# Kernel tuning notes

Hardware: AMD Instinct MI355X
Metric: run time of the kernel (lower is better)

The kernel has to match this reference:

```python
import jax, jax.numpy as jnp
import numpy as np

B, IN, OUT = 128, 1024, 1024
BETA, THRESHOLD, RESET = 0.99, 1.0, 0.8
TAU_POS, TAU_NEG = 20.0, 20.0
A_POS, A_NEG = 0.005, 0.005


def setup_inputs() -> dict:
    key = jax.random.key(0)
    k1, k2, k3, k4, k5 = jax.random.split(key, 5)
    in_spikes = (jax.random.uniform(k1, (B, IN)) < 0.1).astype(jnp.float32)
    # nn.Linear default init: U(-1/sqrt(in), 1/sqrt(in))
    bound = 1.0 / np.sqrt(IN)
    W = jax.random.uniform(k2, (OUT, IN), minval=-bound, maxval=bound, dtype=jnp.float32)
    membrane = jax.random.normal(k3, (B, OUT), dtype=jnp.float32) * 0.5
    # trace timers (time since last spike), random in [0, 50)
    delta_pre = jax.random.uniform(k4, (B, IN), dtype=jnp.float32) * 50.0
    delta_fire = jax.random.uniform(k5, (B, OUT), dtype=jnp.float32) * 50.0
    return {"in_spikes": in_spikes, "W": W, "membrane": membrane,
            "delta_pre": delta_pre, "delta_fire": delta_fire}


def reference(in_spikes, W, membrane, delta_pre, delta_fire):
    # dense projection (bias is unused in the original forward)
    weighted = jnp.matmul(in_spikes, W.T)                      # (B, OUT)
    # LIF neuron
    mem = membrane * BETA + weighted
    spike = (mem > THRESHOLD).astype(jnp.float32)
    mem = jnp.where(spike > 0, mem - RESET, mem)
    # trace updates: increment, reset-to-zero where a spike occurred
    dp = jnp.where(in_spikes > 0, 0.0, delta_pre + 1.0)        # (B, IN)
    df = jnp.where(spike > 0, 0.0, delta_fire + 1.0)           # (B, OUT)
    # pairwise timing difference: (B, IN, OUT)
    delta_t = df[:, None, :] - dp[:, :, None]
    potentiation = (delta_t > 0) * (A_POS * jnp.exp(-delta_t / TAU_POS))
    depression = (delta_t < 0) * (A_NEG * jnp.exp(delta_t / TAU_NEG))
    weight_changes = potentiation - depression                 # (B, IN, OUT)
    avg_weight_changes = weight_changes.mean(axis=0).T         # (OUT, IN)
    new_W = W + avg_weight_changes
    return spike, new_W, mem
```

## Files before the change

### kernel.cpp

```cpp
#include <hip/hip_runtime.h>
#include <cstdint>
#include <cmath>

#define Bb   128
#define INN  1024
#define OUTN 1024
#define A_TOT   (0.005f / 128.0f)
#define INV_TAU (1.0f / 20.0f)

__device__ __forceinline__ uint32_t rne_bf16(float f) {
    uint32_t u = __float_as_uint(f);
    return (u + 0x7fffu + ((u >> 16) & 1u)) >> 16;
}

__global__ __launch_bounds__(256) void transpose_k(const float* __restrict__ W,
                                                   float* __restrict__ Wt) {
    __shared__ float tile[32][33];
    const int bx = blockIdx.x;
    const int by = blockIdx.y;
    const int x = threadIdx.x & 31;
    const int y = threadIdx.x >> 5;
#pragma unroll
    for (int j = 0; j < 4; j++) {
        int o = by * 32 + y + j * 8;
        tile[y + j * 8][x] = W[(size_t)o * INN + bx * 32 + x];
    }
    __syncthreads();
#pragma unroll
    for (int j = 0; j < 4; j++) {
        int i = bx * 32 + y + j * 8;
        Wt[(size_t)i * OUTN + by * 32 + x] = tile[x][y + j * 8];
    }
}

__global__ __launch_bounds__(256) void spmv_lif_pack_k(
    const float* __restrict__ in_spikes, const float* __restrict__ Wt,
    const float* __restrict__ membrane, const float* __restrict__ delta_pre,
    const float* __restrict__ delta_fire,
    uint32_t* __restrict__ OPackB, uint32_t* __restrict__ IPackB,
    float* __restrict__ out_spike, float* __restrict__ out_mem) {
    __shared__ int sIdx[INN];
    __shared__ int sCount;
    const int b = blockIdx.x;
    const int z = blockIdx.y;
    const int t = threadIdx.x;

    if (t < 64) {
        int base = 0;
#pragma unroll
        for (int c = 0; c < 16; c++) {
            float s = in_spikes[(size_t)b * INN + c * 64 + t];
            unsigned long long m = __ballot(s > 0.0f);
            if (s > 0.0f) {
                int pos = base + __popcll(m & ((1ULL << t) - 1ULL));
                sIdx[pos] = c * 64 + t;
            }
            base += __popcll(m);
        }
        if (t == 0) sCount = base;
    }
    __syncthreads();

    const int n = sCount;
    const int o = z * 256 + t;
    float acc = 0.0f;
    int j = 0;
    for (; j + 8 <= n; j += 8) {
        float w0 = Wt[(size_t)sIdx[j + 0] * OUTN + o];
        float w1 = Wt[(size_t)sIdx[j + 1] * OUTN + o];
        float w2 = Wt[(size_t)sIdx[j + 2] * OUTN + o];
        float w3 = Wt[(size_t)sIdx[j + 3] * OUTN + o];
        float w4 = Wt[(size_t)sIdx[j + 4] * OUTN + o];
        float w5 = Wt[(size_t)sIdx[j + 5] * OUTN + o];
        float w6 = Wt[(size_t)sIdx[j + 6] * OUTN + o];
        float w7 = Wt[(size_t)sIdx[j + 7] * OUTN + o];
        acc += ((w0 + w1) + (w2 + w3)) + ((w4 + w5) + (w6 + w7));
    }
    for (; j < n; j++) acc += Wt[(size_t)sIdx[j] * OUTN + o];

    const int n_bo = b * OUTN + o;
    float mem = membrane[n_bo] * 0.99f + acc;
    float s = (mem > 1.0f) ? 1.0f : 0.0f;
    mem = (s > 0.0f) ? mem - 0.8f : mem;
    out_spike[n_bo] = s;
    out_mem[n_bo] = mem;

    float df = (s > 0.0f) ? 0.0f : delta_fire[n_bo] + 1.0f;
    float Oy = expf(-df * INV_TAU);
    float Oz = -A_TOT * expf(df * INV_TAU);
    OPackB[n_bo] = (rne_bf16(Oy) << 16) | rne_bf16(Oz);

    const int n_bi = b * INN + o;
    float sp = in_spikes[n_bi];
    float dp = (sp > 0.0f) ? 0.0f : delta_pre[n_bi] + 1.0f;
    float Iz = expf(-dp * INV_TAU);
    float Iy = A_TOT * expf(dp * INV_TAU);
    IPackB[n_bi] = (rne_bf16(Iz) << 16) | rne_bf16(Iy);
}

__global__ __launch_bounds__(256, 4) void stdp_k(const float* __restrict__ W,
                                                 const uint32_t* __restrict__ OPackB,
                                                 const uint32_t* __restrict__ IPackB,
                                                 float* __restrict__ outW) {
    __shared__ uint32_t sO[32][32];
    __shared__ uint32_t sI[32][32];
    const int t  = threadIdx.x;
    const int o0 = blockIdx.x * 32;
    const int i0 = blockIdx.y * 32;
    const int tx = t & 15;
    const int ty = t >> 4;
    const int srow = t >> 3;
    const int scol = (t & 7) * 4;

    float acc[2][2] = {{0.f, 0.f}, {0.f, 0.f}};

    for (int cb = 0; cb < Bb / 32; cb++) {
        const int bgl = cb * 32 + srow;
        *(uint4*)&sO[srow][scol] =
            *(const uint4*)&OPackB[(size_t)bgl * OUTN + o0 + scol];
        *(uint4*)&sI[srow][scol] =
            *(const uint4*)&IPackB[(size_t)bgl * INN + i0 + scol];
        __syncthreads();
#pragma unroll
        for (int bb = 0; bb < 32; bb++) {
            uint2 po = *(const uint2*)&sO[bb][2 * ty];
            uint2 pi = *(const uint2*)&sI[bb][2 * tx];
#pragma unroll
            for (int a = 0; a < 2; a++) {
                uint32_t o_ = (a == 0) ? po.x : po.y;
#pragma unroll
                for (int c = 0; c < 2; c++) {
                    uint32_t i_ = (c == 0) ? pi.x : pi.y;
                    uint32_t key = min(o_, i_);
                    uint32_t pay = max(o_, i_) << 16;
                    acc[a][c] = fmaf(__uint_as_float(key),
                                     __uint_as_float(pay), acc[a][c]);
                }
            }
        }
        __syncthreads();
    }

#pragma unroll
    for (int a = 0; a < 2; a++) {
        const int o = o0 + 2 * ty + a;
        const size_t off = (size_t)o * INN + i0 + 2 * tx;
        float2 w = *(const float2*)&W[off];
        *(float2*)&outW[off] = make_float2(w.x + acc[a][0], w.y + acc[a][1]);
    }
}

extern "C" void kernel_launch(void* const* d_in, const int* in_sizes, int n_in,
                              void* d_out, int out_size, void* d_ws, size_t ws_size,
                              hipStream_t stream) {
    const float* in_spikes  = (const float*)d_in[0];
    const float* W          = (const float*)d_in[1];
    const float* membrane   = (const float*)d_in[2];
    const float* delta_pre  = (const float*)d_in[3];
    const float* delta_fire = (const float*)d_in[4];

    float* out_spike = (float*)d_out;
    float* out_W     = out_spike + (size_t)Bb * OUTN;
    float* out_mem   = out_W + (size_t)OUTN * INN;

    float* ws        = (float*)d_ws;
    float* Wt        = ws;
    uint32_t* OPackB = (uint32_t*)(Wt + (size_t)INN * OUTN);
    uint32_t* IPackB = OPackB + (size_t)Bb * OUTN;

    hipLaunchKernelGGL(transpose_k, dim3(INN / 32, OUTN / 32), dim3(256), 0, stream,
                       W, Wt);
    hipLaunchKernelGGL(spmv_lif_pack_k, dim3(Bb, 4), dim3(256), 0, stream,
                       in_spikes, Wt, membrane, delta_pre, delta_fire,
                       OPackB, IPackB, out_spike, out_mem);
    hipLaunchKernelGGL(stdp_k, dim3(OUTN / 32, INN / 32), dim3(256), 0, stream,
                       W, OPackB, IPackB, out_W);
}
```

Baseline: 101.5 us.

## Move spike compaction and input packing into transpose kernel; widen STDP tile

The transpose kernel becomes a prep kernel. Besides transposing two tiles per block, it compacts input spike indices into global memory and computes the packed pre-synaptic exponentials, which takes that work off the SpMV/LIF kernel. The STDP kernel now covers a 32x64 tile per block with four accumulators per output row, reusing each loaded O value across more columns and halving the block count. This raises register pressure (launch bounds now allow 2 blocks per SM) and adds global round-trips for the index lists.

New measurement: 101.3 us. About the same (-0.1%).

```diff
diff --git a/kernel.cpp b/kernel.cpp
--- a/kernel.cpp
+++ b/kernel.cpp
@@ -13,39 +13,17 @@
     return (u + 0x7fffu + ((u >> 16) & 1u)) >> 16;
 }
 
-__global__ __launch_bounds__(256) void transpose_k(const float* __restrict__ W,
-                                                   float* __restrict__ Wt) {
+__global__ __launch_bounds__(256) void prep_k(
+    const float* __restrict__ W, const float* __restrict__ in_spikes,
+    const float* __restrict__ delta_pre,
+    float* __restrict__ Wt, uint32_t* __restrict__ IPackB,
+    int* __restrict__ gIdx, int* __restrict__ gCount) {
     __shared__ float tile[32][33];
-    const int bx = blockIdx.x;
-    const int by = blockIdx.y;
-    const int x = threadIdx.x & 31;
-    const int y = threadIdx.x >> 5;
-#pragma unroll
-    for (int j = 0; j < 4; j++) {
-        int o = by * 32 + y + j * 8;
-        tile[y + j * 8][x] = W[(size_t)o * INN + bx * 32 + x];
-    }
-    __syncthreads();
-#pragma unroll
-    for (int j = 0; j < 4; j++) {
-        int i = bx * 32 + y + j * 8;
-        Wt[(size_t)i * OUTN + by * 32 + x] = tile[x][y + j * 8];
-    }
-}
+    const int blk = blockIdx.x;
+    const int t   = threadIdx.x;
 
-__global__ __launch_bounds__(256) void spmv_lif_pack_k(
-    const float* __restrict__ in_spikes, const float* __restrict__ Wt,
-    const float* __restrict__ membrane, const float* __restrict__ delta_pre,
-    const float* __restrict__ delta_fire,
-    uint32_t* __restrict__ OPackB, uint32_t* __restrict__ IPackB,
-    float* __restrict__ out_spike, float* __restrict__ out_mem) {
-    __shared__ int sIdx[INN];
-    __shared__ int sCount;
-    const int b = blockIdx.x;
-    const int z = blockIdx.y;
-    const int t = threadIdx.x;
-
-    if (t < 64) {
+    if ((blk & 3) == 0 && t < 64) {
+        const int b = blk >> 2;
         int base = 0;
 #pragma unroll
         for (int c = 0; c < 16; c++) {
@@ -53,15 +31,52 @@
             unsigned long long m = __ballot(s > 0.0f);
             if (s > 0.0f) {
                 int pos = base + __popcll(m & ((1ULL << t) - 1ULL));
-                sIdx[pos] = c * 64 + t;
+                gIdx[b * INN + pos] = c * 64 + t;
             }
             base += __popcll(m);
         }
-        if (t == 0) sCount = base;
+        if (t == 0) gCount[b] = base;
     }
+
+    {
+        const int e = blk * 256 + t;
+        float sp = in_spikes[e];
+        float dp = (sp > 0.0f) ? 0.0f : delta_pre[e] + 1.0f;
+        float Iz = expf(-dp * INV_TAU);
+        float Iy = A_TOT * expf(dp * INV_TAU);
+        IPackB[e] = (rne_bf16(Iz) << 16) | rne_bf16(Iy);
+    }
+
+    const int x = t & 31, y = t >> 5;
+#pragma unroll
+    for (int k = 0; k < 2; k++) {
+        int tau = blk * 2 + k;
+        int bx = tau & 31, by = tau >> 5;
+        __syncthreads();
+#pragma unroll
+        for (int j = 0; j < 4; j++)
+            tile[y + j * 8][x] = W[(size_t)(by * 32 + y + j * 8) * INN + bx * 32 + x];
+        __syncthreads();
+#pragma unroll
+        for (int j = 0; j < 4; j++)
+            Wt[(size_t)(bx * 32 + y + j * 8) * OUTN + by * 32 + x] = tile[x][y + j * 8];
+    }
+}
+
+__global__ __launch_bounds__(256) void spmv_lif_k(
+    const float* __restrict__ Wt, const float* __restrict__ membrane,
+    const float* __restrict__ delta_fire,
+    const int* __restrict__ gIdx, const int* __restrict__ gCount,
+    uint32_t* __restrict__ OPackB,
+    float* __restrict__ out_spike, float* __restrict__ out_mem) {
+    __shared__ int sIdx[INN];
+    const int b = blockIdx.x;
+    const int z = blockIdx.y;
+    const int t = threadIdx.x;
+    const int n = gCount[b];
+    for (int j = t; j < n; j += 256) sIdx[j] = gIdx[b * INN + j];
     __syncthreads();
 
-    const int n = sCount;
     const int o = z * 256 + t;
     float acc = 0.0f;
     int j = 0;
@@ -89,50 +104,48 @@
     float Oy = expf(-df * INV_TAU);
     float Oz = -A_TOT * expf(df * INV_TAU);
     OPackB[n_bo] = (rne_bf16(Oy) << 16) | rne_bf16(Oz);
-
-    const int n_bi = b * INN + o;
-    float sp = in_spikes[n_bi];
-    float dp = (sp > 0.0f) ? 0.0f : delta_pre[n_bi] + 1.0f;
-    float Iz = expf(-dp * INV_TAU);
-    float Iy = A_TOT * expf(dp * INV_TAU);
-    IPackB[n_bi] = (rne_bf16(Iz) << 16) | rne_bf16(Iy);
 }
 
-__global__ __launch_bounds__(256, 4) void stdp_k(const float* __restrict__ W,
+__global__ __launch_bounds__(256, 2) void stdp_k(const float* __restrict__ W,
                                                  const uint32_t* __restrict__ OPackB,
                                                  const uint32_t* __restrict__ IPackB,
                                                  float* __restrict__ outW) {
     __shared__ uint32_t sO[32][32];
-    __shared__ uint32_t sI[32][32];
+    __shared__ uint32_t sI[32][64];
     const int t  = threadIdx.x;
     const int o0 = blockIdx.x * 32;
-    const int i0 = blockIdx.y * 32;
+    const int i0 = blockIdx.y * 64;
     const int tx = t & 15;
     const int ty = t >> 4;
-    const int srow = t >> 3;
-    const int scol = (t & 7) * 4;
 
-    float acc[2][2] = {{0.f, 0.f}, {0.f, 0.f}};
+    float acc[2][4] = {{0.f,0.f,0.f,0.f},{0.f,0.f,0.f,0.f}};
 
     for (int cb = 0; cb < Bb / 32; cb++) {
-        const int bgl = cb * 32 + srow;
-        *(uint4*)&sO[srow][scol] =
-            *(const uint4*)&OPackB[(size_t)bgl * OUTN + o0 + scol];
-        *(uint4*)&sI[srow][scol] =
-            *(const uint4*)&IPackB[(size_t)bgl * INN + i0 + scol];
+        {
+            const int row = t >> 3, col = (t & 7) * 4;
+            *(uint4*)&sO[row][col] =
+                *(const uint4*)&OPackB[(size_t)(cb * 32 + row) * OUTN + o0 + col];
+        }
+#pragma unroll
+        for (int r = 0; r < 2; r++) {
+            const int idx = r * 256 + t;
+            const int row = idx >> 4, col = (idx & 15) * 4;
+            *(uint4*)&sI[row][col] =
+                *(const uint4*)&IPackB[(size_t)(cb * 32 + row) * INN + i0 + col];
+        }
         __syncthreads();
 #pragma unroll
         for (int bb = 0; bb < 32; bb++) {
             uint2 po = *(const uint2*)&sO[bb][2 * ty];
-            uint2 pi = *(const uint2*)&sI[bb][2 * tx];
+            uint4 pi = *(const uint4*)&sI[bb][4 * tx];
+            uint32_t iv[4] = {pi.x, pi.y, pi.z, pi.w};
 #pragma unroll
             for (int a = 0; a < 2; a++) {
-                uint32_t o_ = (a == 0) ? po.x : po.y;
+                const uint32_t o_ = (a == 0) ? po.x : po.y;
 #pragma unroll
-                for (int c = 0; c < 2; c++) {
-                    uint32_t i_ = (c == 0) ? pi.x : pi.y;
-                    uint32_t key = min(o_, i_);
-                    uint32_t pay = max(o_, i_) << 16;
+                for (int c = 0; c < 4; c++) {
+                    uint32_t key = min(o_, iv[c]);
+                    uint32_t pay = max(o_, iv[c]) << 16;
                     acc[a][c] = fmaf(__uint_as_float(key),
                                      __uint_as_float(pay), acc[a][c]);
                 }
@@ -144,9 +157,11 @@
 #pragma unroll
     for (int a = 0; a < 2; a++) {
         const int o = o0 + 2 * ty + a;
-        const size_t off = (size_t)o * INN + i0 + 2 * tx;
-        float2 w = *(const float2*)&W[off];
-        *(float2*)&outW[off] = make_float2(w.x + acc[a][0], w.y + acc[a][1]);
+        const size_t off = (size_t)o * INN + i0 + 4 * tx;
+        float4 w = *(const float4*)&W[off];
+        float4 r = make_float4(w.x + acc[a][0], w.y + acc[a][1],
+                               w.z + acc[a][2], w.w + acc[a][3]);
+        *(float4*)&outW[off] = r;
     }
 }
 
@@ -167,12 +182,14 @@
     float* Wt        = ws;
     uint32_t* OPackB = (uint32_t*)(Wt + (size_t)INN * OUTN);
     uint32_t* IPackB = OPackB + (size_t)Bb * OUTN;
+    int* gIdx        = (int*)(IPackB + (size_t)Bb * INN);
+    int* gCount      = gIdx + (size_t)Bb * INN;
 
-    hipLaunchKernelGGL(transpose_k, dim3(INN / 32, OUTN / 32), dim3(256), 0, stream,
-                       W, Wt);
-    hipLaunchKernelGGL(spmv_lif_pack_k, dim3(Bb, 4), dim3(256), 0, stream,
-                       in_spikes, Wt, membrane, delta_pre, delta_fire,
-                       OPackB, IPackB, out_spike, out_mem);
-    hipLaunchKernelGGL(stdp_k, dim3(OUTN / 32, INN / 32), dim3(256), 0, stream,
+    hipLaunchKernelGGL(prep_k, dim3(512), dim3(256), 0, stream,
+                       W, in_spikes, delta_pre, Wt, IPackB, gIdx, gCount);
+    hipLaunchKernelGGL(spmv_lif_k, dim3(Bb, 4), dim3(256), 0, stream,
+                       Wt, membrane, delta_fire, gIdx, gCount,
+                       OPackB, out_spike, out_mem);
+    hipLaunchKernelGGL(stdp_k, dim3(OUTN / 32, INN / 64), dim3(256), 0, stream,
                        W, OPackB, IPackB, out_W);
 }
```
